# Performance work log

Hardware: AMD Instinct MI355X
Metric: run time of the kernel (lower is better)

## Reference

```python
import jax, jax.numpy as jnp
import numpy as np

B, N, DIM = 4, 2048, 1024
HEADS, DIM_HEAD = 16, 64
INNER = HEADS * DIM_HEAD  # 1024
SCALE = DIM_HEAD ** -0.5

def setup_inputs() -> dict:
    key = jax.random.key(0)
    k1, k2, k3 = jax.random.split(key, 3)
    x = jax.random.normal(k1, (B, N, DIM), dtype=jnp.float32)
    w_qkv = jax.random.normal(k2, (DIM, 3 * INNER), dtype=jnp.float32) * (DIM ** -0.5)
    w_out = jax.random.normal(k3, (INNER, DIM), dtype=jnp.float32) * (INNER ** -0.5)
    b_out = jnp.zeros((DIM,), dtype=jnp.float32)
    return {"x": x, "w_qkv": w_qkv, "w_out": w_out, "b_out": b_out}

def reference(x, w_qkv, w_out, b_out):
    b, n, _ = x.shape
    qkv = x @ w_qkv  # [b, n, 3*inner]
    q, k, v = jnp.split(qkv, 3, axis=-1)
    # [b, n, h, d] -> [b, h, n, d]
    reshape = lambda t: t.reshape(b, n, HEADS, DIM_HEAD).transpose(0, 2, 1, 3)
    q, k, v = reshape(q), reshape(k), reshape(v)
    dots = jnp.einsum('bhqd,bhkd->bhqk', q, k) * SCALE
    attn = jax.nn.softmax(dots, axis=-1)
    out = jnp.einsum('bhqk,bhkd->bhqd', attn, v)
    out = out.transpose(0, 2, 1, 3).reshape(b, n, INNER)
    return out @ w_out + b_out
```

## Files before the change

kernel.cpp:

```cpp
#include <hip/hip_runtime.h>

typedef unsigned short u16;
typedef __bf16 bf16_t;
typedef bf16_t bf16x8 __attribute__((ext_vector_type(8)));
typedef float f32x4 __attribute__((ext_vector_type(4)));
typedef float f32x16 __attribute__((ext_vector_type(16)));
typedef u16 u16x8 __attribute__((ext_vector_type(8)));
typedef u16 u16x4 __attribute__((ext_vector_type(4)));
typedef unsigned uint2v __attribute__((ext_vector_type(2)));

#define B_     4
#define N_     2048
#define DIM_   1024
#define HEADS_ 16
#define DH_    64
#define INNER_ 1024
#define QKV3_  3072
#define SCALE_ 0.125f
#define LOG2E_ 1.44269504089f

__device__ __forceinline__ u16 f2bf(float f) {
  union { float f; unsigned u; } v; v.f = f;
  unsigned r = v.u + 0x7FFFu + ((v.u >> 16) & 1u);
  return (u16)(r >> 16);
}
__device__ __forceinline__ u16 bfbits(float f) {
  bf16_t b = (bf16_t)f;
  return __builtin_bit_cast(u16, b);
}
__device__ __forceinline__ unsigned packbf(float lo, float hi) {
  return (unsigned)bfbits(lo) | ((unsigned)bfbits(hi) << 16);
}

#if __has_builtin(__builtin_amdgcn_exp2f)
#define EXP2F(x) __builtin_amdgcn_exp2f(x)
#else
#define EXP2F(x) __expf((x) * 0.69314718056f)
#endif

typedef __attribute__((address_space(1))) const unsigned int ga_u32;
typedef __attribute__((address_space(3))) unsigned int ls_u32;
__device__ __forceinline__ void gload16(const void* g, void* l) {
  __builtin_amdgcn_global_load_lds((ga_u32*)g, (ls_u32*)l, 16, 0, 0);
}

__global__ __launch_bounds__(256) void cvt_f32_bf16(const float* __restrict__ in,
                                                    u16* __restrict__ out, int n8) {
  int i = blockIdx.x * 256 + threadIdx.x;
  if (i < n8) {
    const float4* p = (const float4*)(in + (size_t)i * 8);
    float4 a = p[0], b = p[1];
    u16x8 o;
    o[0] = f2bf(a.x); o[1] = f2bf(a.y); o[2] = f2bf(a.z); o[3] = f2bf(a.w);
    o[4] = f2bf(b.x); o[5] = f2bf(b.y); o[6] = f2bf(b.z); o[7] = f2bf(b.w);
    *(u16x8*)(out + (size_t)i * 8) = o;
  }
}

__global__ __launch_bounds__(256) void transp_w(const float* __restrict__ in,
                                                u16* __restrict__ out, int Kd, int Nd) {
  __shared__ float t[32][33];
  int n0 = blockIdx.x * 32, k0 = blockIdx.y * 32;
  int tx = threadIdx.x & 31, ty = threadIdx.x >> 5;
#pragma unroll
  for (int i = 0; i < 4; i++)
    t[ty + i * 8][tx] = in[(size_t)(k0 + ty + i * 8) * Nd + n0 + tx];
  __syncthreads();
#pragma unroll
  for (int i = 0; i < 4; i++)
    out[(size_t)(n0 + ty + i * 8) * Kd + k0 + tx] = f2bf(t[tx][ty + i * 8]);
}

__global__ __launch_bounds__(256) void ktile_prep(const u16* __restrict__ qkv,
                                                  u16* __restrict__ ktiled) {
  const int blk = blockIdx.x;
  const int bh = blk >> 5, kt = blk & 31;
  const int b = bh >> 4, h = bh & 15;
  const int tid = threadIdx.x;
  const int s = tid & 7, r0 = tid >> 3;
  const u16* src = qkv + (size_t)(b * N_ + kt * 64 + r0) * QKV3_ + INNER_ + h * DH_ + s * 8;
  u16* dst = ktiled + (size_t)blk * 4096 + s * 512 + r0 * 8;
  uint4 v0 = *(const uint4*)(src);
  uint4 v1 = *(const uint4*)(src + (size_t)32 * QKV3_);
  *(uint4*)(dst) = v0;
  *(uint4*)(dst + 256) = v1;
}

__global__ __launch_bounds__(256) void transp_v(const u16* __restrict__ qkv,
                                                u16* __restrict__ vtiled) {
  __shared__ u16 t[32][33];
  int bh = blockIdx.z; int b = bh >> 4, h = bh & 15;
  int n0 = blockIdx.x * 32, d0 = blockIdx.y * 32;
  int tx = threadIdx.x & 31, ty = threadIdx.x >> 5;
#pragma unroll
  for (int i = 0; i < 4; i++)
    t[ty + i * 8][tx] =
        qkv[(size_t)(b * N_ + n0 + ty + i * 8) * QKV3_ + 2 * INNER_ + h * DH_ + d0 + tx];
  __syncthreads();
  const int n = n0 + tx;
  u16* obase = vtiled + (size_t)bh * 131072 + (size_t)(n >> 6) * 4096 +
               ((n >> 3) & 7) * 512 + (n & 7);
#pragma unroll
  for (int i = 0; i < 4; i++)
    obase[(d0 + ty + i * 8) * 8] = t[tx][ty + i * 8];
}

template <int F32OUT>
__global__ __launch_bounds__(256) void gemm_bt(const u16* __restrict__ A,
                                               const u16* __restrict__ BT,
                                               void* __restrict__ Cp,
                                               const float* __restrict__ bias,
                                               int M, int N, int K) {
  __shared__ alignas(16) u16 ldsA[2][128 * 64];
  __shared__ alignas(16) u16 ldsB[2][128 * 64];
  const int tid = threadIdx.x;
  const int lane = tid & 63, wid = tid >> 6;
  const int l16 = lane & 15, lg = lane >> 4;

  int bid = blockIdx.x;
  const int cpx = gridDim.x >> 3;
  bid = (bid & 7) * cpx + (bid >> 3);

  const int ntiles = N >> 7;
  const int tm = bid / ntiles, tn = bid % ntiles;
  const int m0 = tm << 7, n0 = tn << 7;
  const int wr = wid >> 1, wc = wid & 1;

  const int srow_in = lane >> 3;
  const int soff = ((lane & 7) ^ srow_in) * 8;

  f32x4 acc[4][4];
#pragma unroll
  for (int i = 0; i < 4; i++)
#pragma unroll
    for (int j = 0; j < 4; j++) acc[i][j] = f32x4{0.f, 0.f, 0.f, 0.f};

  const int KSTEPS = K >> 6;

#define GSTAGE_(kk, buf)                                                           \
  do {                                                                             \
    const int k1_ = (kk) << 6;                                                     \
    char* bA_ = (char*)&ldsA[(buf)][0];                                            \
    char* bB_ = (char*)&ldsB[(buf)][0];                                            \
    _Pragma("unroll")                                                              \
    for (int i_ = 0; i_ < 4; i_++) {                                               \
      const int rb_ = wid * 32 + i_ * 8;                                           \
      gload16(A  + (size_t)(m0 + rb_ + srow_in) * K + k1_ + soff, bA_ + rb_ * 128);\
      gload16(BT + (size_t)(n0 + rb_ + srow_in) * K + k1_ + soff, bB_ + rb_ * 128);\
    }                                                                              \
  } while (0)

  GSTAGE_(0, 0);
  GSTAGE_(1, 1);

  for (int ks = 0; ks < KSTEPS; ks++) {
    if (ks + 1 < KSTEPS) asm volatile("s_waitcnt vmcnt(8)" ::: "memory");
    else                 asm volatile("s_waitcnt vmcnt(0)" ::: "memory");
    __builtin_amdgcn_s_barrier();

    const char* cA = (const char*)&ldsA[ks & 1][0];
    const char* cB = (const char*)&ldsB[ks & 1][0];

    bf16x8 bf[4][2];
#pragma unroll
    for (int n = 0; n < 4; n++) {
      int row = wc * 64 + n * 16 + l16;
      int rb = row * 128, swz = (row & 7) << 4;
      bf[n][0] = *(const bf16x8*)(cB + rb + ((lg * 16) ^ swz));
      bf[n][1] = *(const bf16x8*)(cB + rb + ((64 + lg * 16) ^ swz));
    }
    __builtin_amdgcn_s_setprio(1);
#pragma unroll
    for (int mm = 0; mm < 4; mm++) {
      int row = wr * 64 + mm * 16 + l16;
      int rb = row * 128, swz = (row & 7) << 4;
      bf16x8 af0 = *(const bf16x8*)(cA + rb + ((lg * 16) ^ swz));
      bf16x8 af1 = *(const bf16x8*)(cA + rb + ((64 + lg * 16) ^ swz));
#pragma unroll
      for (int n = 0; n < 4; n++) {
        acc[mm][n] = __builtin_amdgcn_mfma_f32_16x16x32_bf16(af0, bf[n][0], acc[mm][n], 0, 0, 0);
        acc[mm][n] = __builtin_amdgcn_mfma_f32_16x16x32_bf16(af1, bf[n][1], acc[mm][n], 0, 0, 0);
      }
    }
    __builtin_amdgcn_s_setprio(0);

    __builtin_amdgcn_s_barrier();
    if (ks + 2 < KSTEPS) GSTAGE_(ks + 2, ks & 1);
  }
#undef GSTAGE_

#pragma unroll
  for (int mm = 0; mm < 4; mm++) {
#pragma unroll
    for (int n = 0; n < 4; n++) {
      int row = m0 + wr * 64 + mm * 16 + lg * 4;
      int col = n0 + wc * 64 + n * 16 + l16;
#pragma unroll
      for (int j = 0; j < 4; j++) {
        if (F32OUT)
          ((float*)Cp)[(size_t)(row + j) * N + col] = acc[mm][n][j] + bias[col];
        else
          ((u16*)Cp)[(size_t)(row + j) * N + col] = f2bf(acc[mm][n][j]);
      }
    }
  }
}

__global__ __launch_bounds__(512, 4) void attn_fwd(const u16* __restrict__ qkv,
                                                   const u16* __restrict__ ktiled,
                                                   const u16* __restrict__ vtiled,
                                                   u16* __restrict__ abuf) {
  __shared__ alignas(16) u16 ldsK[3][64 * 64];
  __shared__ alignas(16) u16 ldsV[3][64 * 64];

  const int tid = threadIdx.x;
  const int lane = tid & 63, wid = tid >> 6;
  const int l32 = lane & 31, hl = lane >> 5;

  int bid = blockIdx.x;
  bid = (bid & 7) * 64 + (bid >> 3);
  const int bh = bid >> 3, qt = bid & 7;
  const int b = bh >> 4, h = bh & 15;
  const int q0 = qt * 256 + wid * 32;

  constexpr float QS = SCALE_ * LOG2E_;
  bf16x8 qf[4];
  {
    const u16* qrow = qkv + (size_t)(b * N_ + q0 + l32) * QKV3_ + h * DH_ + hl * 8;
#pragma unroll
    for (int step = 0; step < 4; step++) {
      bf16x8 t = *(const bf16x8*)(qrow + step * 16);
#pragma unroll
      for (int i = 0; i < 8; i++) t[i] = (bf16_t)((float)t[i] * QS);
      qf[step] = t;
    }
  }

  const u16* kts = ktiled + (size_t)bh * 131072 + tid * 8;
  const u16* vts = vtiled + (size_t)bh * 131072 + tid * 8;
  const int sdst = wid << 10;

  const int kofs = (hl << 10) + (l32 << 4);

  float lrow = 0.f;
  f32x16 acc[2];
#pragma unroll
  for (int i = 0; i < 16; i++) { acc[0][i] = 0.f; acc[1][i] = 0.f; }

  gload16(kts, (char*)ldsK + sdst);
  gload16(vts, (char*)ldsV + sdst);
  gload16(kts + 4096, (char*)ldsK + 8192 + sdst);
  gload16(vts + 4096, (char*)ldsV + 8192 + sdst);

  const int NT = N_ / 64;
  int cur = 0, pre = 2;

  for (int kt = 0; kt < NT; ++kt) {
    if (kt < NT - 1) asm volatile("s_waitcnt vmcnt(2)" ::: "memory");
    else             asm volatile("s_waitcnt vmcnt(0)" ::: "memory");
    __builtin_amdgcn_s_barrier();
    if (kt + 2 < NT) {
      gload16(kts + (size_t)(kt + 2) * 4096, (char*)ldsK + pre * 8192 + sdst);
      gload16(vts + (size_t)(kt + 2) * 4096, (char*)ldsV + pre * 8192 + sdst);
    }

    const char* Kb = (const char*)ldsK + cur * 8192;
    const char* Vb = (const char*)ldsV + cur * 8192;

    f32x16 s[2];
    __builtin_amdgcn_s_setprio(1);
#pragma unroll
    for (int ktile = 0; ktile < 2; ktile++) {
      f32x16 c;
#pragma unroll
      for (int i = 0; i < 16; i++) c[i] = 0.f;
      const char* rb = Kb + (ktile << 9) + kofs;
#pragma unroll
      for (int step = 0; step < 4; step++) {
        bf16x8 kf = *(const bf16x8*)(rb + (step << 11));
        c = __builtin_amdgcn_mfma_f32_32x32x16_bf16(kf, qf[step], c, 0, 0, 0);
      }
      s[ktile] = c;
    }
    __builtin_amdgcn_s_setprio(0);

    float ps0 = 0.f, ps1 = 0.f;
#pragma unroll
    for (int ktile = 0; ktile < 2; ktile++)
#pragma unroll
      for (int i = 0; i < 16; i += 2) {
        const float p0 = EXP2F(s[ktile][i]);
        const float p1 = EXP2F(s[ktile][i + 1]);
        s[ktile][i] = p0; s[ktile][i + 1] = p1;
        ps0 += p0; ps1 += p1;
      }
    lrow += ps0 + ps1;

    bf16x8 pb[4];
#pragma unroll
    for (int ktile = 0; ktile < 2; ktile++)
#pragma unroll
      for (int par = 0; par < 2; par++) {
        const int rb8 = par * 8;
        const unsigned c0 = packbf(s[ktile][rb8 + 0], s[ktile][rb8 + 1]);
        const unsigned c1 = packbf(s[ktile][rb8 + 2], s[ktile][rb8 + 3]);
        const unsigned c2 = packbf(s[ktile][rb8 + 4], s[ktile][rb8 + 5]);
        const unsigned c3 = packbf(s[ktile][rb8 + 6], s[ktile][rb8 + 7]);
        const uint2v r02 = __builtin_amdgcn_permlane32_swap(c0, c2, false, false);
        const uint2v r13 = __builtin_amdgcn_permlane32_swap(c1, c3, false, false);
        union { unsigned u[4]; bf16x8 v; } w;
        w.u[0] = r02[0]; w.u[1] = r13[0]; w.u[2] = r02[1]; w.u[3] = r13[1];
        pb[ktile * 2 + par] = w.v;
      }

    __builtin_amdgcn_s_setprio(1);
#pragma unroll
    for (int dtile = 0; dtile < 2; dtile++) {
      const char* rb = Vb + (dtile << 9) + kofs;
      f32x16 c = acc[dtile];
#pragma unroll
      for (int step = 0; step < 4; step++) {
        bf16x8 vf = *(const bf16x8*)(rb + (step << 11));
        c = __builtin_amdgcn_mfma_f32_32x32x16_bf16(vf, pb[step], c, 0, 0, 0);
      }
      acc[dtile] = c;
    }
    __builtin_amdgcn_s_setprio(0);

    cur = (cur == 2) ? 0 : cur + 1;
    pre = (pre == 2) ? 0 : pre + 1;
  }

  lrow += __shfl_xor(lrow, 32);
  const float inv = 1.f / lrow;
  const size_t row = (size_t)(b * N_ + q0 + l32);
#pragma unroll
  for (int dtile = 0; dtile < 2; dtile++)
#pragma unroll
    for (int g = 0; g < 4; g++) {
      u16x4 w;
#pragma unroll
      for (int j = 0; j < 4; j++) w[j] = bfbits(acc[dtile][g * 4 + j] * inv);
      const int d = dtile * 32 + g * 8 + hl * 4;
      *(u16x4*)(abuf + row * INNER_ + h * DH_ + d) = w;
    }
}

extern "C" void kernel_launch(void* const* d_in, const int* in_sizes, int n_in,
                              void* d_out, int out_size, void* d_ws, size_t ws_size,
                              hipStream_t stream) {
  const float* x     = (const float*)d_in[0];
  const float* w_qkv = (const float*)d_in[1];
  const float* w_out = (const float*)d_in[2];
  const float* b_out = (const float*)d_in[3];
  float* out = (float*)d_out;

  char* ws = (char*)d_ws;
  u16* xb     = (u16*)(ws);
  u16* wqkvT  = (u16*)(ws + (size_t)(16 << 20));
  u16* woutT  = (u16*)(ws + (size_t)(22 << 20));
  u16* qkv    = (u16*)(ws + (size_t)(24 << 20));
  u16* vtiled = (u16*)(ws + (size_t)(72 << 20));
  u16* ktiled = (u16*)d_out;
  u16* abuf   = xb;

  cvt_f32_bf16<<<4096, 256, 0, stream>>>(x, xb, (B_ * N_ * DIM_) / 8);
  transp_w<<<dim3(QKV3_ / 32, DIM_ / 32), 256, 0, stream>>>(w_qkv, wqkvT, DIM_, QKV3_);
  transp_w<<<dim3(DIM_ / 32, INNER_ / 32), 256, 0, stream>>>(w_out, woutT, INNER_, DIM_);
  gemm_bt<0><<<(B_ * N_ / 128) * (QKV3_ / 128), 256, 0, stream>>>(
      xb, wqkvT, qkv, nullptr, B_ * N_, QKV3_, DIM_);
  ktile_prep<<<B_ * HEADS_ * 32, 256, 0, stream>>>(qkv, ktiled);
  transp_v<<<dim3(N_ / 32, DH_ / 32, B_ * HEADS_), 256, 0, stream>>>(qkv, vtiled);
  attn_fwd<<<512, 512, 0, stream>>>(qkv, ktiled, vtiled, abuf);
  gemm_bt<1><<<(B_ * N_ / 128) * (DIM_ / 128), 256, 0, stream>>>(
      abuf, woutT, out, b_out, B_ * N_, DIM_, INNER_);
}
```

Before: 200.7 us.

## Fuse K/V tiling into QKV GEMM epilogue and drop separate prep kernels

The QKV projection GEMM now writes Q to a compact buffer and scatters K and V directly into the tiled layouts the attention kernel consumes. This removes the ktile_prep and transp_v kernels, along with their extra read and write of the K and V data and two launches. In exchange, the epilogue stores become scattered 2-byte writes with poorer coalescing, especially for the V layout, which is transposed along the sequence dimension.

New measurement: 189.6 us (median of 2 runs). 5.5% less time.

```diff
diff --git a/kernel.cpp b/kernel.cpp
--- a/kernel.cpp
+++ b/kernel.cpp
@@ -71,46 +71,12 @@
     out[(size_t)(n0 + ty + i * 8) * Kd + k0 + tx] = f2bf(t[tx][ty + i * 8]);
 }
 
-__global__ __launch_bounds__(256) void ktile_prep(const u16* __restrict__ qkv,
-                                                  u16* __restrict__ ktiled) {
-  const int blk = blockIdx.x;
-  const int bh = blk >> 5, kt = blk & 31;
-  const int b = bh >> 4, h = bh & 15;
-  const int tid = threadIdx.x;
-  const int s = tid & 7, r0 = tid >> 3;
-  const u16* src = qkv + (size_t)(b * N_ + kt * 64 + r0) * QKV3_ + INNER_ + h * DH_ + s * 8;
-  u16* dst = ktiled + (size_t)blk * 4096 + s * 512 + r0 * 8;
-  uint4 v0 = *(const uint4*)(src);
-  uint4 v1 = *(const uint4*)(src + (size_t)32 * QKV3_);
-  *(uint4*)(dst) = v0;
-  *(uint4*)(dst + 256) = v1;
-}
-
-__global__ __launch_bounds__(256) void transp_v(const u16* __restrict__ qkv,
-                                                u16* __restrict__ vtiled) {
-  __shared__ u16 t[32][33];
-  int bh = blockIdx.z; int b = bh >> 4, h = bh & 15;
-  int n0 = blockIdx.x * 32, d0 = blockIdx.y * 32;
-  int tx = threadIdx.x & 31, ty = threadIdx.x >> 5;
-#pragma unroll
-  for (int i = 0; i < 4; i++)
-    t[ty + i * 8][tx] =
-        qkv[(size_t)(b * N_ + n0 + ty + i * 8) * QKV3_ + 2 * INNER_ + h * DH_ + d0 + tx];
-  __syncthreads();
-  const int n = n0 + tx;
-  u16* obase = vtiled + (size_t)bh * 131072 + (size_t)(n >> 6) * 4096 +
-               ((n >> 3) & 7) * 512 + (n & 7);
-#pragma unroll
-  for (int i = 0; i < 4; i++)
-    obase[(d0 + ty + i * 8) * 8] = t[tx][ty + i * 8];
-}
-
-template <int F32OUT>
-__global__ __launch_bounds__(256) void gemm_bt(const u16* __restrict__ A,
-                                               const u16* __restrict__ BT,
-                                               void* __restrict__ Cp,
-                                               const float* __restrict__ bias,
-                                               int M, int N, int K) {
+__global__ __launch_bounds__(256) void gemm_qkv(const u16* __restrict__ A,
+                                                const u16* __restrict__ BT,
+                                                u16* __restrict__ qbuf,
+                                                u16* __restrict__ ktiled,
+                                                u16* __restrict__ vtiled,
+                                                int M, int N, int K) {
   __shared__ alignas(16) u16 ldsA[2][128 * 64];
   __shared__ alignas(16) u16 ldsB[2][128 * 64];
   const int tid = threadIdx.x;
@@ -189,6 +155,125 @@
   }
 #undef GSTAGE_
 
+  const int seg = n0 >> 10;
+#pragma unroll
+  for (int mm = 0; mm < 4; mm++) {
+#pragma unroll
+    for (int nn = 0; nn < 4; nn++) {
+      const int row = m0 + wr * 64 + mm * 16 + lg * 4;
+      const int col = n0 + wc * 64 + nn * 16 + l16;
+      if (seg == 0) {
+#pragma unroll
+        for (int j = 0; j < 4; j++)
+          qbuf[(size_t)(row + j) * INNER_ + col] = f2bf(acc[mm][nn][j]);
+      } else if (seg == 1) {
+        const int kd = col - 1024;
+        const int h = kd >> 6, s = (kd >> 3) & 7, e = kd & 7;
+#pragma unroll
+        for (int j = 0; j < 4; j++) {
+          const int rr = row + j;
+          const int b = rr >> 11, n = rr & (N_ - 1);
+          ktiled[(((size_t)(b * HEADS_ + h) * 32 + (n >> 6)) << 12) +
+                 (s << 9) + ((n & 63) << 3) + e] = f2bf(acc[mm][nn][j]);
+        }
+      } else {
+        const int vd = col - 2048;
+        const int h = vd >> 6, d = vd & 63;
+#pragma unroll
+        for (int j = 0; j < 4; j++) {
+          const int rr = row + j;
+          const int b = rr >> 11, n = rr & (N_ - 1);
+          vtiled[(((size_t)(b * HEADS_ + h) * 32 + (n >> 6)) << 12) +
+                 (((n >> 3) & 7) << 9) + (d << 3) + (n & 7)] = f2bf(acc[mm][nn][j]);
+        }
+      }
+    }
+  }
+}
+
+__global__ __launch_bounds__(256) void gemm_bt(const u16* __restrict__ A,
+                                               const u16* __restrict__ BT,
+                                               float* __restrict__ Cp,
+                                               const float* __restrict__ bias,
+                                               int M, int N, int K) {
+  __shared__ alignas(16) u16 ldsA[2][128 * 64];
+  __shared__ alignas(16) u16 ldsB[2][128 * 64];
+  const int tid = threadIdx.x;
+  const int lane = tid & 63, wid = tid >> 6;
+  const int l16 = lane & 15, lg = lane >> 4;
+
+  int bid = blockIdx.x;
+  const int cpx = gridDim.x >> 3;
+  bid = (bid & 7) * cpx + (bid >> 3);
+
+  const int ntiles = N >> 7;
+  const int tm = bid / ntiles, tn = bid % ntiles;
+  const int m0 = tm << 7, n0 = tn << 7;
+  const int wr = wid >> 1, wc = wid & 1;
+
+  const int srow_in = lane >> 3;
+  const int soff = ((lane & 7) ^ srow_in) * 8;
+
+  f32x4 acc[4][4];
+#pragma unroll
+  for (int i = 0; i < 4; i++)
+#pragma unroll
+    for (int j = 0; j < 4; j++) acc[i][j] = f32x4{0.f, 0.f, 0.f, 0.f};
+
+  const int KSTEPS = K >> 6;
+
+#define GSTAGE_(kk, buf)                                                           \
+  do {                                                                             \
+    const int k1_ = (kk) << 6;                                                     \
+    char* bA_ = (char*)&ldsA[(buf)][0];                                            \
+    char* bB_ = (char*)&ldsB[(buf)][0];                                            \
+    _Pragma("unroll")                                                              \
+    for (int i_ = 0; i_ < 4; i_++) {                                               \
+      const int rb_ = wid * 32 + i_ * 8;                                           \
+      gload16(A  + (size_t)(m0 + rb_ + srow_in) * K + k1_ + soff, bA_ + rb_ * 128);\
+      gload16(BT + (size_t)(n0 + rb_ + srow_in) * K + k1_ + soff, bB_ + rb_ * 128);\
+    }                                                                              \
+  } while (0)
+
+  GSTAGE_(0, 0);
+  GSTAGE_(1, 1);
+
+  for (int ks = 0; ks < KSTEPS; ks++) {
+    if (ks + 1 < KSTEPS) asm volatile("s_waitcnt vmcnt(8)" ::: "memory");
+    else                 asm volatile("s_waitcnt vmcnt(0)" ::: "memory");
+    __builtin_amdgcn_s_barrier();
+
+    const char* cA = (const char*)&ldsA[ks & 1][0];
+    const char* cB = (const char*)&ldsB[ks & 1][0];
+
+    bf16x8 bf[4][2];
+#pragma unroll
+    for (int n = 0; n < 4; n++) {
+      int row = wc * 64 + n * 16 + l16;
+      int rb = row * 128, swz = (row & 7) << 4;
+      bf[n][0] = *(const bf16x8*)(cB + rb + ((lg * 16) ^ swz));
+      bf[n][1] = *(const bf16x8*)(cB + rb + ((64 + lg * 16) ^ swz));
+    }
+    __builtin_amdgcn_s_setprio(1);
+#pragma unroll
+    for (int mm = 0; mm < 4; mm++) {
+      int row = wr * 64 + mm * 16 + l16;
+      int rb = row * 128, swz = (row & 7) << 4;
+      bf16x8 af0 = *(const bf16x8*)(cA + rb + ((lg * 16) ^ swz));
+      bf16x8 af1 = *(const bf16x8*)(cA + rb + ((64 + lg * 16) ^ swz));
+#pragma unroll
+      for (int n = 0; n < 4; n++) {
+        acc[mm][n] = __builtin_amdgcn_mfma_f32_16x16x32_bf16(af0, bf[n][0], acc[mm][n], 0, 0, 0);
+        acc[mm][n] = __builtin_amdgcn_mfma_f32_16x16x32_bf16(af1, bf[n][1], acc[mm][n], 0, 0, 0);
+      }
+    }
+    __builtin_amdgcn_s_setprio(0);
+
+    __builtin_amdgcn_s_barrier();
+    if (ks + 2 < KSTEPS) GSTAGE_(ks + 2, ks & 1);
+  }
+#undef GSTAGE_
+
 #pragma unroll
   for (int mm = 0; mm < 4; mm++) {
 #pragma unroll
@@ -196,17 +281,13 @@
       int row = m0 + wr * 64 + mm * 16 + lg * 4;
       int col = n0 + wc * 64 + n * 16 + l16;
 #pragma unroll
-      for (int j = 0; j < 4; j++) {
-        if (F32OUT)
-          ((float*)Cp)[(size_t)(row + j) * N + col] = acc[mm][n][j] + bias[col];
-        else
-          ((u16*)Cp)[(size_t)(row + j) * N + col] = f2bf(acc[mm][n][j]);
-      }
-    }
-  }
-}
-
-__global__ __launch_bounds__(512, 4) void attn_fwd(const u16* __restrict__ qkv,
+      for (int j = 0; j < 4; j++)
+        Cp[(size_t)(row + j) * N + col] = acc[mm][n][j] + bias[col];
+    }
+  }
+}
+
+__global__ __launch_bounds__(512, 4) void attn_fwd(const u16* __restrict__ qbuf,
                                                    const u16* __restrict__ ktiled,
                                                    const u16* __restrict__ vtiled,
                                                    u16* __restrict__ abuf) {
@@ -226,7 +307,7 @@
   constexpr float QS = SCALE_ * LOG2E_;
   bf16x8 qf[4];
   {
-    const u16* qrow = qkv + (size_t)(b * N_ + q0 + l32) * QKV3_ + h * DH_ + hl * 8;
+    const u16* qrow = qbuf + (size_t)(b * N_ + q0 + l32) * INNER_ + h * DH_ + hl * 8;
 #pragma unroll
     for (int step = 0; step < 4; step++) {
       bf16x8 t = *(const bf16x8*)(qrow + step * 16);
@@ -359,19 +440,17 @@
   u16* xb     = (u16*)(ws);
   u16* wqkvT  = (u16*)(ws + (size_t)(16 << 20));
   u16* woutT  = (u16*)(ws + (size_t)(22 << 20));
-  u16* qkv    = (u16*)(ws + (size_t)(24 << 20));
-  u16* vtiled = (u16*)(ws + (size_t)(72 << 20));
-  u16* ktiled = (u16*)d_out;
+  u16* qbuf   = (u16*)(ws + (size_t)(24 << 20));
+  u16* ktiled = (u16*)(ws + (size_t)(40 << 20));
+  u16* vtiled = (u16*)(ws + (size_t)(56 << 20));
   u16* abuf   = xb;
 
   cvt_f32_bf16<<<4096, 256, 0, stream>>>(x, xb, (B_ * N_ * DIM_) / 8);
   transp_w<<<dim3(QKV3_ / 32, DIM_ / 32), 256, 0, stream>>>(w_qkv, wqkvT, DIM_, QKV3_);
   transp_w<<<dim3(DIM_ / 32, INNER_ / 32), 256, 0, stream>>>(w_out, woutT, INNER_, DIM_);
-  gemm_bt<0><<<(B_ * N_ / 128) * (QKV3_ / 128), 256, 0, stream>>>(
-      xb, wqkvT, qkv, nullptr, B_ * N_, QKV3_, DIM_);
-  ktile_prep<<<B_ * HEADS_ * 32, 256, 0, stream>>>(qkv, ktiled);
-  transp_v<<<dim3(N_ / 32, DH_ / 32, B_ * HEADS_), 256, 0, stream>>>(qkv, vtiled);
-  attn_fwd<<<512, 512, 0, stream>>>(qkv, ktiled, vtiled, abuf);
-  gemm_bt<1><<<(B_ * N_ / 128) * (DIM_ / 128), 256, 0, stream>>>(
+  gemm_qkv<<<(B_ * N_ / 128) * (QKV3_ / 128), 256, 0, stream>>>(
+      xb, wqkvT, qbuf, ktiled, vtiled, B_ * N_, QKV3_, DIM_);
+  attn_fwd<<<512, 512, 0, stream>>>(qbuf, ktiled, vtiled, abuf);
+  gemm_bt<<<(B_ * N_ / 128) * (DIM_ / 128), 256, 0, stream>>>(
       abuf, woutT, out, b_out, B_ * N_, DIM_, INNER_);
 }
```
